# Optimization experiments

Hardware: AMD Instinct MI355X
Metric: run time of the kernel (lower is better)

## Reference

```python
import jax, jax.numpy as jnp
import numpy as np
from jax import lax

EPS = 1e-5
NUM_HEADS = 8


def _safe_norm(x):
    # sqrt(max(sum x^2, EPS^2)) == max(||x||, EPS); grad-safe at 0
    return jnp.sqrt(jnp.maximum(jnp.sum(x * x, axis=-1, keepdims=True), EPS * EPS))


def _project(x):
    norm = _safe_norm(x)
    max_norm = 1.0 - EPS
    scale = jnp.where(norm >= max_norm, max_norm / (norm + EPS), jnp.ones_like(norm))
    return x * scale


def _logmap0(y):
    # logarithmic_map(0, y): lambda_0 = 2/(1+EPS)
    y = _project(y)
    n = _safe_norm(y)  # clamp(min=EPS) is built in
    lam = 2.0 / (1.0 + EPS)
    return (2.0 / lam) * jnp.arctanh(n) * (y / n)


def _expmap0(v):
    # exponential_map(0, v): lambda_0 = 2/(1+EPS)
    n = _safe_norm(v)
    lam = 2.0 / (1.0 + EPS)
    return _project(jnp.tanh(lam * n / 2.0) * (v / n))


def _mobius_add(x, y):
    x = _project(x)
    y = _project(y)
    xy = jnp.sum(x * y, axis=-1, keepdims=True)
    xn = jnp.sum(x * x, axis=-1, keepdims=True)
    yn = jnp.sum(y * y, axis=-1, keepdims=True)
    num = (1.0 + 2.0 * xy + yn) * x + (1.0 - xn) * y
    den = 1.0 + 2.0 * xy + xn * yn + EPS
    return _project(num / den)


def _hyp_linear(x, W, b):
    # HyperbolicLinear.forward: project -> logmap0 -> linear -> expmap0 -> mobius-add bias
    x = _project(x)
    xt = _logmap0(x)
    t = xt @ W.T
    r = _expmap0(t)
    r = _mobius_add(r, jnp.broadcast_to(b, r.shape))
    return r


def setup_inputs() -> dict:
    key = jax.random.key(0)
    ks = jax.random.split(key, 11)
    B, S, E = 4, 512, 512

    def xavier(k, shape):
        bound = np.sqrt(6.0 / (shape[0] + shape[1]))
        return jax.random.uniform(k, shape, jnp.float32, -bound, bound)

    return {
        "query": jax.random.normal(ks[0], (B, S, E), jnp.float32),
        "key": jax.random.normal(ks[1], (B, S, E), jnp.float32),
        "value": jax.random.normal(ks[2], (B, S, E), jnp.float32),
        "Wq": xavier(ks[3], (E, E)), "bq": 0.01 * jax.random.normal(ks[4], (E,), jnp.float32),
        "Wk": xavier(ks[5], (E, E)), "bk": 0.01 * jax.random.normal(ks[6], (E,), jnp.float32),
        "Wv": xavier(ks[7], (E, E)), "bv": 0.01 * jax.random.normal(ks[8], (E,), jnp.float32),
        "Wo": xavier(ks[9], (E, E)), "bo": 0.01 * jax.random.normal(ks[10], (E,), jnp.float32),
    }


def reference(query, key, value, Wq, bq, Wk, bk, Wv, bv, Wo, bo):
    B, S, E = query.shape
    H = NUM_HEADS
    D = E // H

    Q = _hyp_linear(query, Wq, bq).reshape(B, S, H, D).transpose(0, 2, 1, 3)  # [B,H,S,D]
    K = _hyp_linear(key, Wk, bk).reshape(B, S, H, D).transpose(0, 2, 1, 3)
    V = _hyp_linear(value, Wv, bv).reshape(B, S, H, D).transpose(0, 2, 1, 3)

    # Pairwise Poincare distance: d(q,k) = acosh(1 + 2||q-k||^2/((1-|q|^2)(1-|k|^2)) + EPS)
    q = _project(Q)
    k = _project(K)
    qn = jnp.sum(q * q, axis=-1)  # [B,H,S]
    kn = jnp.sum(k * k, axis=-1)  # [B,H,S]
    qk = jnp.einsum('bhqd,bhkd->bhqk', q, k)
    num = jnp.maximum(qn[..., :, None] + kn[..., None, :] - 2.0 * qk, 0.0)
    den = jnp.maximum((1.0 - qn)[..., :, None] * (1.0 - kn)[..., None, :], EPS)
    dist = jnp.arccosh(1.0 + 2.0 * num / den + EPS)  # [B,H,Sq,Sk]
    attn = jax.nn.softmax(-dist, axis=-1)

    # Sequential Mobius-add accumulation over key/value positions
    wt = jnp.moveaxis(attn, 3, 0)  # [Sk,B,H,Sq]
    vt = jnp.moveaxis(V, 2, 0)     # [Sk,B,H,D]

    @jax.checkpoint
    def step(ws, wv):
        wj, vj = wv  # wj: [B,H,Sq], vj: [B,H,D]
        return _mobius_add(ws, wj[..., None] * vj[:, :, None, :]), None

    ws0 = jnp.zeros((B, H, S, D), query.dtype)
    attended, _ = lax.scan(step, ws0, (wt, vt))  # [B,H,Sq,D]

    attended = attended.transpose(0, 2, 1, 3).reshape(B, S, E)
    return _hyp_linear(attended, Wo, bo)
```

## Files before the change

kernel.cpp:

```cpp
#include <hip/hip_runtime.h>
#include <math.h>

#define EPS  1e-5f
#define EPS2 1e-10f
#define MAXN (1.0f - EPS)

using short8  = __attribute__((ext_vector_type(8))) short;
using floatx4 = __attribute__((ext_vector_type(4))) float;
using float2v = __attribute__((ext_vector_type(2))) float;

template <int CTRL>
static __device__ __forceinline__ float qperm(float x) {
  return __int_as_float(__builtin_amdgcn_update_dpp(
      __float_as_int(x), __float_as_int(x), CTRL, 0xF, 0xF, false));
}
#define QP_XOR1    0xB1
#define QP_XOR2    0x4E
#define QP_HALFMIR 0x141

#if __has_builtin(__builtin_elementwise_fma)
static __device__ __forceinline__ float2v fma2(float2v a, float2v b, float2v c) {
  return __builtin_elementwise_fma(a, b, c);
}
#else
static __device__ __forceinline__ float2v fma2(float2v a, float2v b, float2v c) {
  float2v r; r.x = fmaf(a.x, b.x, c.x); r.y = fmaf(a.y, b.y, c.y); return r;
}
#endif

static __device__ __forceinline__ int pack_hi2(float a, float b) {
  return (int)((__float_as_uint(a) >> 16) | (__float_as_uint(b) & 0xFFFF0000u));
}
static __device__ __forceinline__ float hi_of(float a) {
  return __uint_as_float(__float_as_uint(a) & 0xFFFF0000u);
}

static __device__ __forceinline__ float logmap_f(float ss) {
  const float r = sqrtf(fmaxf(ss, EPS2));
  float at;
  if (r >= MAXN) {
    at = 0.5f * logf((r * (2.0f - EPS) + EPS) / (EPS * (1.0f + r)));
  } else {
    at = 0.5f * logf((1.0f + r) / (1.0f - r));
  }
  return (1.0f + EPS) * at / r;
}

__global__ __launch_bounds__(256) void k_gemm_mfma(
    const float* __restrict__ A0, const float* __restrict__ A1, const float* __restrict__ A2,
    const float* __restrict__ W0, const float* __restrict__ W1, const float* __restrict__ W2,
    float* __restrict__ Cbase) {
  const int z = blockIdx.z;
  const float* A = (z == 0) ? A0 : ((z == 1) ? A1 : A2);
  const float* W = (z == 0) ? W0 : ((z == 1) ? W1 : W2);
  float* C = Cbase + (size_t)z * (2048 * 512);
  __shared__ int Ahi[64][36], Alo[64][36], Whi[64][36], Wlo[64][36];
  __shared__ float f_lds[64];
  const int t = threadIdx.x;
  const int n0 = blockIdx.x * 64;
  const int m0 = blockIdx.y * 64;
  const int row = t >> 2, c0 = (t & 3) * 16, ci = (t & 3) * 8;
  const int w = t >> 6, lane = t & 63;
  const int quad = lane >> 4, l16 = lane & 15;
  const int mw = (w & 1) * 32, nw = (w >> 1) * 32;
  floatx4 acc[2][2];
#pragma unroll
  for (int i = 0; i < 2; ++i)
#pragma unroll
    for (int j = 0; j < 2; ++j) acc[i][j] = (floatx4){0.f, 0.f, 0.f, 0.f};
  float ssq = 0.0f;

  for (int k0 = 0; k0 < 512; k0 += 64) {
    float4 av[4], wv[4];
#pragma unroll
    for (int i = 0; i < 4; ++i) {
      av[i] = *(const float4*)&A[(size_t)(n0 + row) * 512 + k0 + c0 + 4 * i];
      wv[i] = *(const float4*)&W[(size_t)(m0 + row) * 512 + k0 + c0 + 4 * i];
    }
    int pAh[8], pAl[8], pWh[8], pWl[8];
#pragma unroll
    for (int i = 0; i < 4; ++i) {
      ssq = fmaf(av[i].x, av[i].x, ssq); ssq = fmaf(av[i].y, av[i].y, ssq);
      ssq = fmaf(av[i].z, av[i].z, ssq); ssq = fmaf(av[i].w, av[i].w, ssq);
      pAh[2 * i]     = pack_hi2(av[i].x, av[i].y);
      pAh[2 * i + 1] = pack_hi2(av[i].z, av[i].w);
      pAl[2 * i]     = pack_hi2(av[i].x - hi_of(av[i].x), av[i].y - hi_of(av[i].y));
      pAl[2 * i + 1] = pack_hi2(av[i].z - hi_of(av[i].z), av[i].w - hi_of(av[i].w));
      pWh[2 * i]     = pack_hi2(wv[i].x, wv[i].y);
      pWh[2 * i + 1] = pack_hi2(wv[i].z, wv[i].w);
      pWl[2 * i]     = pack_hi2(wv[i].x - hi_of(wv[i].x), wv[i].y - hi_of(wv[i].y));
      pWl[2 * i + 1] = pack_hi2(wv[i].z - hi_of(wv[i].z), wv[i].w - hi_of(wv[i].w));
    }
    __syncthreads();
    *(int4*)&Ahi[row][ci]     = *(int4*)&pAh[0];
    *(int4*)&Ahi[row][ci + 4] = *(int4*)&pAh[4];
    *(int4*)&Alo[row][ci]     = *(int4*)&pAl[0];
    *(int4*)&Alo[row][ci + 4] = *(int4*)&pAl[4];
    *(int4*)&Whi[row][ci]     = *(int4*)&pWh[0];
    *(int4*)&Whi[row][ci + 4] = *(int4*)&pWh[4];
    *(int4*)&Wlo[row][ci]     = *(int4*)&pWl[0];
    *(int4*)&Wlo[row][ci + 4] = *(int4*)&pWl[4];
    __syncthreads();
#pragma unroll
    for (int kk = 0; kk < 64; kk += 32) {
      short8 ah[2], al[2], bh[2], bl[2];
#pragma unroll
      for (int i = 0; i < 2; ++i) {
        ah[i] = *(const short8*)&((const short*)Ahi[mw + i * 16 + l16])[kk + quad * 8];
        al[i] = *(const short8*)&((const short*)Alo[mw + i * 16 + l16])[kk + quad * 8];
        bh[i] = *(const short8*)&((const short*)Whi[nw + i * 16 + l16])[kk + quad * 8];
        bl[i] = *(const short8*)&((const short*)Wlo[nw + i * 16 + l16])[kk + quad * 8];
      }
#pragma unroll
      for (int i = 0; i < 2; ++i)
#pragma unroll
        for (int j = 0; j < 2; ++j) {
          acc[i][j] = __builtin_amdgcn_mfma_f32_16x16x32_bf16(ah[i], bh[j], acc[i][j], 0, 0, 0);
          acc[i][j] = __builtin_amdgcn_mfma_f32_16x16x32_bf16(ah[i], bl[j], acc[i][j], 0, 0, 0);
          acc[i][j] = __builtin_amdgcn_mfma_f32_16x16x32_bf16(al[i], bh[j], acc[i][j], 0, 0, 0);
        }
    }
  }
  ssq += qperm<QP_XOR1>(ssq);
  ssq += qperm<QP_XOR2>(ssq);
  if ((t & 3) == 0) f_lds[row] = logmap_f(ssq);
  __syncthreads();
#pragma unroll
  for (int i = 0; i < 2; ++i) {
    const int lrow_base = mw + i * 16 + quad * 4;
#pragma unroll
    for (int r = 0; r < 4; ++r) {
      const float fv = f_lds[lrow_base + r];
#pragma unroll
      for (int j = 0; j < 2; ++j)
        C[(size_t)(n0 + lrow_base + r) * 512 + m0 + nw + j * 16 + l16] = fv * acc[i][j][r];
    }
  }
}

__global__ __launch_bounds__(256) void k_post(const float* __restrict__ tin,
                                              const float* __restrict__ b0,
                                              const float* __restrict__ b1,
                                              const float* __restrict__ b2,
                                              float* __restrict__ o0, float* __restrict__ o1,
                                              float* __restrict__ o2,
                                              float* __restrict__ nrm0, float* __restrict__ nrm1,
                                              float* __restrict__ nrm2,
                                              float* __restrict__ rowsum_init, int final_mode) {
  const int nrow = blockIdx.x, z = blockIdx.y, t = threadIdx.x;
  const float* tv = tin + ((size_t)z * 2048 + nrow) * 512;
  const float* bias = (z == 0) ? b0 : ((z == 1) ? b1 : b2);
  const int e0 = 2 * t;
  const float2 tp = *(const float2*)&tv[e0];
  const float2 bp = *(const float2*)&bias[e0];
  float p_tt = tp.x * tp.x + tp.y * tp.y;
  float p_tb = tp.x * bp.x + tp.y * bp.y;
  float p_bb = bp.x * bp.x + bp.y * bp.y;
#pragma unroll
  for (int m = 32; m; m >>= 1) {
    p_tt += __shfl_xor(p_tt, m, 64);
    p_tb += __shfl_xor(p_tb, m, 64);
    p_bb += __shfl_xor(p_bb, m, 64);
  }
  __shared__ float red[4][3];
  const int lane = t & 63, w = t >> 6;
  if (lane == 0) { red[w][0] = p_tt; red[w][1] = p_tb; red[w][2] = p_bb; }
  __syncthreads();
  const float s_tt = red[0][0] + red[1][0] + red[2][0] + red[3][0];
  const float s_tb = red[0][1] + red[1][1] + red[2][1] + red[3][1];
  const float s_bb = red[0][2] + red[1][2] + red[2][2] + red[3][2];
  const float tn = sqrtf(fmaxf(s_tt, EPS2));
  const float th = tanhf(tn / (1.0f + EPS));
  const float g = th / tn;
  const float rnorm = th * (sqrtf(s_tt) / tn);
  const float sr = (rnorm >= MAXN) ? (MAXN / (rnorm + EPS)) : 1.0f;
  const float gr = g * sr;
  const float rn = (rnorm * sr) * (rnorm * sr);
  const float bnorm = sqrtf(fmaxf(s_bb, EPS2));
  const float sb = (bnorm >= MAXN) ? (MAXN / (bnorm + EPS)) : 1.0f;
  const float xy = gr * sb * s_tb;
  const float yn = (sb * sb) * s_bb;
  const float Af = 1.0f + 2.0f * xy + yn;
  const float Cf = 1.0f - rn;
  const float den = 1.0f + 2.0f * xy + rn * yn + EPS;
  const float id = 1.0f / den;
  const float on_raw = (Af * Af * rn + 2.0f * Af * Cf * xy + Cf * Cf * yn) * (id * id);
  const float no = sqrtf(fmaxf(on_raw, EPS2));
  const float so = (no >= MAXN) ? (MAXN / (no + EPS)) : 1.0f;
  const float ms = id * so;
  const float ca = gr * Af * ms;
  const float cb = sb * Cf * ms;
  const float v0 = ca * tp.x + cb * bp.x;
  const float v1 = ca * tp.y + cb * bp.y;
  if (final_mode) {
    float2 o; o.x = v0; o.y = v1;
    *(float2*)&o0[(size_t)nrow * 512 + e0] = o;
    return;
  }
  float hp = v0 * v0 + v1 * v1;
#pragma unroll
  for (int m = 16; m; m >>= 1) hp += __shfl_xor(hp, m, 64);
  const float hnr = sqrtf(fmaxf(hp, EPS2));
  float sh = 1.0f;
  if (z != 2) sh = (hnr >= MAXN) ? (MAXN / (hnr + EPS)) : 1.0f;
  float* outz = (z == 0) ? o0 : ((z == 1) ? o1 : o2);
  float* nz = (z == 0) ? nrm0 : ((z == 1) ? nrm1 : nrm2);
  const int b = nrow >> 9, s = nrow & 511, h = e0 >> 6, d = e0 & 63;
  float2 o; o.x = v0 * sh; o.y = v1 * sh;
  *(float2*)&outz[(((size_t)(b * 8 + h) * 512 + s) * 64 + d)] = o;
  if ((t & 31) == 0) nz[(size_t)(b * 8 + h) * 512 + s] = hp * sh * sh;
  if (z == 0 && t < 8) rowsum_init[((size_t)(nrow >> 9) * 8 + t) * 512 + (nrow & 511)] = 0.0f;
}

__global__ __launch_bounds__(256) void k_logits(const float* __restrict__ Q,
                                                const float* __restrict__ K,
                                                const float* __restrict__ qn,
                                                const float* __restrict__ kn,
                                                float* __restrict__ attn,
                                                float* __restrict__ rowsum) {
  const int bh = blockIdx.z;
  const int i0 = blockIdx.x * 64;
  const int j0 = blockIdx.y * 64;
  const float* Qb = Q + (size_t)bh * 512 * 64;
  const float* Kb = K + (size_t)bh * 512 * 64;
  __shared__ int Qhi[64][36], Qlo[64][36], Khi[64][36], Klo[64][36];
  const int t = threadIdx.x;
  const int row = t >> 2, c0 = (t & 3) * 16, ci = (t & 3) * 8;
  const int w = t >> 6, lane = t & 63;
  const int quad = lane >> 4, l16 = lane & 15;
  const int mw = (w & 1) * 32, nw = (w >> 1) * 32;
  float4 qv4[4], kv4[4];
#pragma unroll
  for (int i = 0; i < 4; ++i) {
    qv4[i] = *(const float4*)&Qb[(size_t)(i0 + row) * 64 + c0 + 4 * i];
    kv4[i] = *(const float4*)&Kb[(size_t)(j0 + row) * 64 + c0 + 4 * i];
  }
  int pQh[8], pQl[8], pKh[8], pKl[8];
#pragma unroll
  for (int i = 0; i < 4; ++i) {
    pQh[2 * i]     = pack_hi2(qv4[i].x, qv4[i].y);
    pQh[2 * i + 1] = pack_hi2(qv4[i].z, qv4[i].w);
    pQl[2 * i]     = pack_hi2(qv4[i].x - hi_of(qv4[i].x), qv4[i].y - hi_of(qv4[i].y));
    pQl[2 * i + 1] = pack_hi2(qv4[i].z - hi_of(qv4[i].z), qv4[i].w - hi_of(qv4[i].w));
    pKh[2 * i]     = pack_hi2(kv4[i].x, kv4[i].y);
    pKh[2 * i + 1] = pack_hi2(kv4[i].z, kv4[i].w);
    pKl[2 * i]     = pack_hi2(kv4[i].x - hi_of(kv4[i].x), kv4[i].y - hi_of(kv4[i].y));
    pKl[2 * i + 1] = pack_hi2(kv4[i].z - hi_of(kv4[i].z), kv4[i].w - hi_of(kv4[i].w));
  }
  *(int4*)&Qhi[row][ci]     = *(int4*)&pQh[0];
  *(int4*)&Qhi[row][ci + 4] = *(int4*)&pQh[4];
  *(int4*)&Qlo[row][ci]     = *(int4*)&pQl[0];
  *(int4*)&Qlo[row][ci + 4] = *(int4*)&pQl[4];
  *(int4*)&Khi[row][ci]     = *(int4*)&pKh[0];
  *(int4*)&Khi[row][ci + 4] = *(int4*)&pKh[4];
  *(int4*)&Klo[row][ci]     = *(int4*)&pKl[0];
  *(int4*)&Klo[row][ci + 4] = *(int4*)&pKl[4];
  __syncthreads();
  floatx4 acc[2][2];
#pragma unroll
  for (int i = 0; i < 2; ++i)
#pragma unroll
    for (int j = 0; j < 2; ++j) acc[i][j] = (floatx4){0.f, 0.f, 0.f, 0.f};
#pragma unroll
  for (int kk = 0; kk < 64; kk += 32) {
    short8 ah[2], al[2], bhv[2], blv[2];
#pragma unroll
    for (int i = 0; i < 2; ++i) {
      ah[i]  = *(const short8*)&((const short*)Qhi[mw + i * 16 + l16])[kk + quad * 8];
      al[i]  = *(const short8*)&((const short*)Qlo[mw + i * 16 + l16])[kk + quad * 8];
      bhv[i] = *(const short8*)&((const short*)Khi[nw + i * 16 + l16])[kk + quad * 8];
      blv[i] = *(const short8*)&((const short*)Klo[nw + i * 16 + l16])[kk + quad * 8];
    }
#pragma unroll
    for (int i = 0; i < 2; ++i)
#pragma unroll
      for (int j = 0; j < 2; ++j) {
        acc[i][j] = __builtin_amdgcn_mfma_f32_16x16x32_bf16(ah[i], bhv[j], acc[i][j], 0, 0, 0);
        acc[i][j] = __builtin_amdgcn_mfma_f32_16x16x32_bf16(ah[i], blv[j], acc[i][j], 0, 0, 0);
        acc[i][j] = __builtin_amdgcn_mfma_f32_16x16x32_bf16(al[i], bhv[j], acc[i][j], 0, 0, 0);
      }
  }
#pragma unroll
  for (int i = 0; i < 2; ++i) {
    float rs_acc[4] = {0.f, 0.f, 0.f, 0.f};
#pragma unroll
    for (int r = 0; r < 4; ++r) {
      const int grow = i0 + mw + i * 16 + quad * 4 + r;
      const float qni = qn[(size_t)bh * 512 + grow];
      const float rq = 1.0f - qni;
#pragma unroll
      for (int j = 0; j < 2; ++j) {
        const int gcol = j0 + nw + j * 16 + l16;
        const float knj = kn[(size_t)bh * 512 + gcol];
        const float num = fmaxf(qni + knj - 2.0f * acc[i][j][r], 0.0f);
        const float den = fmaxf(rq * (1.0f - knj), EPS);
        const float wv = fmaf(2.0f * num, __builtin_amdgcn_rcpf(den), EPS);
        const float s_ = 1.0f + wv + sqrtf(wv * (wv + 2.0f));
        const float rr = __builtin_amdgcn_rcpf(s_);
        rs_acc[r] += rr;
        attn[((size_t)bh * 512 + grow) * 512 + gcol] = rr;
      }
    }
#pragma unroll
    for (int r = 0; r < 4; ++r) {
      float v = rs_acc[r];
      v += __shfl_xor(v, 1, 64); v += __shfl_xor(v, 2, 64);
      v += __shfl_xor(v, 4, 64); v += __shfl_xor(v, 8, 64);
      if (l16 == 0)
        atomicAdd(&rowsum[(size_t)bh * 512 + i0 + mw + i * 16 + quad * 4 + r], v);
    }
  }
}

__global__ __launch_bounds__(256) void k_scan(const float* __restrict__ V,
                                              const float* __restrict__ vn,
                                              const float* __restrict__ rw,
                                              const float* __restrict__ rowsum,
                                              float* __restrict__ att) {
  __shared__ __align__(16) float v_lds[64 * 64];
  __shared__ __align__(16) float swyn_lds[64 * 66];
  __shared__ float g_lds[64];
  const int blk = blockIdx.x;
  const int bh = blk >> 4;
  const int i0 = (blk & 15) * 32;
  const int t = threadIdx.x;
  const int lane = t & 63, w = t >> 6;
  const int row_blk = w * 8 + (lane >> 3);
  const int sub = lane & 7;
  const int d0 = sub * 8;
  const float* Vb = V + (size_t)bh * 512 * 64;
  const float* vnb = vn + (size_t)bh * 512;
  const float* arow = rw + ((size_t)bh * 512 + i0 + row_blk) * 512;
  const float inv_s = __builtin_amdgcn_rcpf(rowsum[(size_t)bh * 512 + i0 + row_blk]);

  float2v wsv[4];
#pragma unroll
  for (int k = 0; k < 4; ++k) wsv[k] = (float2v){0.f, 0.f};
  float xn = 0.0f;

  for (int jc = 0; jc < 512; jc += 64) {
#pragma unroll
    for (int it = 0; it < 4; ++it) {
      const int idx4 = it * 256 + t;
      *(float4*)&v_lds[idx4 * 4] = *(const float4*)&Vb[(size_t)jc * 64 + idx4 * 4];
    }
    const float4 a0 = *(const float4*)&arow[jc + sub * 8];
    const float4 a1 = *(const float4*)&arow[jc + sub * 8 + 4];
    const float4 n0 = *(const float4*)&vnb[jc + sub * 8];
    const float4 n1 = *(const float4*)&vnb[jc + sub * 8 + 4];
    const float wq[8] = {a0.x, a0.y, a0.z, a0.w, a1.x, a1.y, a1.z, a1.w};
    const float nq[8] = {n0.x, n0.y, n0.z, n0.w, n1.x, n1.y, n1.z, n1.w};
#pragma unroll
    for (int e = 0; e < 8; ++e) {
      const float wgt = wq[e] * inv_s;
      float2 p; p.x = wgt; p.y = (wgt * wgt) * nq[e];
      *(float2*)&swyn_lds[(sub * 8 + e) * 66 + row_blk * 2] = p;
    }
    __syncthreads();

    {
      const int jg = row_blk * 2;
      const float4 va0 = *(const float4*)&v_lds[jg * 64 + d0];
      const float4 va1 = *(const float4*)&v_lds[jg * 64 + d0 + 4];
      const float4 vb0 = *(const float4*)&v_lds[(jg + 1) * 64 + d0];
      const float4 vb1 = *(const float4*)&v_lds[(jg + 1) * 64 + d0 + 4];
      const float4 vc0 = *(const float4*)&v_lds[((jg + 2) & 63) * 64 + d0];
      const float4 vc1 = *(const float4*)&v_lds[((jg + 2) & 63) * 64 + d0 + 4];
      float p0 = va0.x * vb0.x + va0.y * vb0.y + va0.z * vb0.z + va0.w * vb0.w +
                 va1.x * vb1.x + va1.y * vb1.y + va1.z * vb1.z + va1.w * vb1.w;
      float p1 = vb0.x * vc0.x + vb0.y * vc0.y + vb0.z * vc0.z + vb0.w * vc0.w +
                 vb1.x * vc1.x + vb1.y * vc1.y + vb1.z * vc1.z + vb1.w * vc1.w;
      p0 += qperm<QP_XOR1>(p0); p0 += qperm<QP_XOR2>(p0); p0 += qperm<QP_HALFMIR>(p0);
      p1 += qperm<QP_XOR1>(p1); p1 += qperm<QP_XOR2>(p1); p1 += qperm<QP_HALFMIR>(p1);
      if (sub == 0) { g_lds[jg] = p0; g_lds[jg + 1] = p1; }
    }
    float2v vcur[4];
    {
      const float4 c0v = *(const float4*)&v_lds[d0];
      const float4 c1v = *(const float4*)&v_lds[d0 + 4];
      vcur[0] = (float2v){c0v.x, c0v.y}; vcur[1] = (float2v){c0v.z, c0v.w};
      vcur[2] = (float2v){c1v.x, c1v.y}; vcur[3] = (float2v){c1v.z, c1v.w};
    }
    float2v dd = wsv[0] * vcur[0];
    dd = fma2(wsv[1], vcur[1], dd);
    dd = fma2(wsv[2], vcur[2], dd);
    dd = fma2(wsv[3], vcur[3], dd);
    float D = dd.x + dd.y;
    D += qperm<QP_XOR1>(D); D += qperm<QP_XOR2>(D); D += qperm<QP_HALFMIR>(D);
    __syncthreads();

#pragma unroll
    for (int j = 0; j < 64; ++j) {
      const float2 sy2 = *(const float2*)&swyn_lds[j * 66 + row_blk * 2];
      const float sw = sy2.x, yn = sy2.y;
      const float xnyn1 = fmaf(xn, yn, 1.0f + EPS);
      const float sxy   = xn + yn;
      const float ynp1  = 1.0f + yn;
      const float Cfsw  = (1.0f - xn) * sw;
      float2v vnx[4];
      float E = 0.0f;
      if (j < 63) {
        const float4 nx0 = *(const float4*)&v_lds[(j + 1) * 64 + d0];
        const float4 nx1 = *(const float4*)&v_lds[(j + 1) * 64 + d0 + 4];
        vnx[0] = (float2v){nx0.x, nx0.y}; vnx[1] = (float2v){nx0.z, nx0.w};
        vnx[2] = (float2v){nx1.x, nx1.y}; vnx[3] = (float2v){nx1.z, nx1.w};
        float2v ee = wsv[0] * vnx[0];
        ee = fma2(wsv[1], vnx[1], ee);
        ee = fma2(wsv[2], vnx[2], ee);
        ee = fma2(wsv[3], vnx[3], ee);
        E = ee.x + ee.y;
        E += qperm<QP_XOR1>(E); E += qperm<QP_XOR2>(E); E += qperm<QP_HALFMIR>(E);
      }
      const float xy  = sw * D;
      const float den = fmaf(2.0f, xy, xnyn1);
      const float s2  = fmaf(2.0f, xy, sxy);
      const float Af  = fmaf(2.0f, xy, ynp1);
      const float id  = __builtin_amdgcn_rcpf(den);
      const float dn  = den - EPS;
      const float am  = Af * id;
      const float cm  = Cfsw * id;
      xn = (s2 * id) * (dn * id);
      const float2v amv = {am, am};
      const float2v cmv = {cm, cm};
      wsv[0] = fma2(amv, wsv[0], cmv * vcur[0]);
      wsv[1] = fma2(amv, wsv[1], cmv * vcur[1]);
      wsv[2] = fma2(amv, wsv[2], cmv * vcur[2]);
      wsv[3] = fma2(amv, wsv[3], cmv * vcur[3]);
      if (j < 63) {
        D = fmaf(am, E, cm * g_lds[j]);
        vcur[0] = vnx[0]; vcur[1] = vnx[1]; vcur[2] = vnx[2]; vcur[3] = vnx[3];
      }
    }
    __syncthreads();
  }
  const int b = bh >> 3, h = bh & 7;
  float* o = att + (((size_t)b * 512 + i0 + row_blk) * 512 + h * 64 + d0);
  float4 s0; s0.x = wsv[0].x; s0.y = wsv[0].y; s0.z = wsv[1].x; s0.w = wsv[1].y;
  float4 s1; s1.x = wsv[2].x; s1.y = wsv[2].y; s1.z = wsv[3].x; s1.w = wsv[3].y;
  *(float4*)&o[0] = s0;
  *(float4*)&o[4] = s1;
}

extern "C" void kernel_launch(void* const* d_in, const int* in_sizes, int n_in,
                              void* d_out, int out_size, void* d_ws, size_t ws_size,
                              hipStream_t stream) {
  const float* query = (const float*)d_in[0];
  const float* key_  = (const float*)d_in[1];
  const float* value = (const float*)d_in[2];
  const float* Wq = (const float*)d_in[3];
  const float* bq = (const float*)d_in[4];
  const float* Wk = (const float*)d_in[5];
  const float* bk = (const float*)d_in[6];
  const float* Wv = (const float*)d_in[7];
  const float* bv = (const float*)d_in[8];
  const float* Wo = (const float*)d_in[9];
  const float* bo = (const float*)d_in[10];
  float* ws = (float*)d_ws;
  const size_t M = 1u << 20;
  float* Qb     = ws;
  float* Kb     = ws + 1 * M;
  float* Vb     = ws + 2 * M;
  float* qn     = ws + 3 * M;
  float* kn     = qn + 16384;
  float* vn     = kn + 16384;
  float* rowsum = vn + 16384;
  float* rw     = ws + 4 * M;
  float* t3     = ws + 12 * M;
  float* att    = ws + 15 * M;
  float* to_    = ws + 16 * M;

  k_gemm_mfma<<<dim3(32, 8, 3), 256, 0, stream>>>(query, key_, value, Wq, Wk, Wv, t3);
  k_post<<<dim3(2048, 3), 256, 0, stream>>>(t3, bq, bk, bv, Qb, Kb, Vb, qn, kn, vn,
                                            rowsum, 0);
  k_logits<<<dim3(8, 8, 32), 256, 0, stream>>>(Qb, Kb, qn, kn, rw, rowsum);
  k_scan<<<512, 256, 0, stream>>>(Vb, vn, rw, rowsum, att);
  k_gemm_mfma<<<dim3(32, 8, 1), 256, 0, stream>>>(att, att, att, Wo, Wo, Wo, to_);
  k_post<<<dim3(2048, 1), 256, 0, stream>>>(to_, bo, bo, bo, (float*)d_out,
                                            nullptr, nullptr, nullptr, nullptr, nullptr,
                                            nullptr, 1);
}
```

Measured before the change: 239.9 us.

## Fuse all six stages into one cooperative persistent kernel with grid syncs

Replaces the six separate kernel launches with a single cooperative kernel of 512 blocks. Each stage runs as a grid-stride loop over its original block indices, stages are separated by grid.sync, and one shared-memory buffer is reused across stages. This removes per-launch overhead and the gaps between kernels. In exchange, occupancy is capped by the largest stage's shared memory, the grid is fixed at 512 blocks, grid-wide barriers are added, and correctness depends on all blocks being co-resident.

```diff
diff --git a/kernel.cpp b/kernel.cpp
--- a/kernel.cpp
+++ b/kernel.cpp
@@ -1,5 +1,8 @@
 #include <hip/hip_runtime.h>
+#include <hip/hip_cooperative_groups.h>
 #include <math.h>
+
+namespace cg = cooperative_groups;
 
 #define EPS  1e-5f
 #define EPS2 1e-10f
@@ -46,19 +49,14 @@
   return (1.0f + EPS) * at / r;
 }
 
-__global__ __launch_bounds__(256) void k_gemm_mfma(
-    const float* __restrict__ A0, const float* __restrict__ A1, const float* __restrict__ A2,
-    const float* __restrict__ W0, const float* __restrict__ W1, const float* __restrict__ W2,
-    float* __restrict__ Cbase) {
-  const int z = blockIdx.z;
-  const float* A = (z == 0) ? A0 : ((z == 1) ? A1 : A2);
-  const float* W = (z == 0) ? W0 : ((z == 1) ? W1 : W2);
-  float* C = Cbase + (size_t)z * (2048 * 512);
-  __shared__ int Ahi[64][36], Alo[64][36], Whi[64][36], Wlo[64][36];
-  __shared__ float f_lds[64];
+struct SGemm { int Ahi[64][36]; int Alo[64][36]; int Whi[64][36]; int Wlo[64][36]; float f_lds[64]; };
+struct SLog  { int Qhi[64][36]; int Qlo[64][36]; int Khi[64][36]; int Klo[64][36]; };
+struct SScan { float v_lds[64 * 64]; float swyn[64 * 66]; float g[64]; };
+struct SPost { float red[4][3]; };
+
+static __device__ void gemm_body(const float* __restrict__ A, const float* __restrict__ W,
+                                 float* __restrict__ C, int n0, int m0, SGemm* S) {
   const int t = threadIdx.x;
-  const int n0 = blockIdx.x * 64;
-  const int m0 = blockIdx.y * 64;
   const int row = t >> 2, c0 = (t & 3) * 16, ci = (t & 3) * 8;
   const int w = t >> 6, lane = t & 63;
   const int quad = lane >> 4, l16 = lane & 15;
@@ -92,24 +90,24 @@
       pWl[2 * i + 1] = pack_hi2(wv[i].z - hi_of(wv[i].z), wv[i].w - hi_of(wv[i].w));
     }
     __syncthreads();
-    *(int4*)&Ahi[row][ci]     = *(int4*)&pAh[0];
-    *(int4*)&Ahi[row][ci + 4] = *(int4*)&pAh[4];
-    *(int4*)&Alo[row][ci]     = *(int4*)&pAl[0];
-    *(int4*)&Alo[row][ci + 4] = *(int4*)&pAl[4];
-    *(int4*)&Whi[row][ci]     = *(int4*)&pWh[0];
-    *(int4*)&Whi[row][ci + 4] = *(int4*)&pWh[4];
-    *(int4*)&Wlo[row][ci]     = *(int4*)&pWl[0];
-    *(int4*)&Wlo[row][ci + 4] = *(int4*)&pWl[4];
+    *(int4*)&S->Ahi[row][ci]     = *(int4*)&pAh[0];
+    *(int4*)&S->Ahi[row][ci + 4] = *(int4*)&pAh[4];
+    *(int4*)&S->Alo[row][ci]     = *(int4*)&pAl[0];
+    *(int4*)&S->Alo[row][ci + 4] = *(int4*)&pAl[4];
+    *(int4*)&S->Whi[row][ci]     = *(int4*)&pWh[0];
+    *(int4*)&S->Whi[row][ci + 4] = *(int4*)&pWh[4];
+    *(int4*)&S->Wlo[row][ci]     = *(int4*)&pWl[0];
+    *(int4*)&S->Wlo[row][ci + 4] = *(int4*)&pWl[4];
     __syncthreads();
 #pragma unroll
     for (int kk = 0; kk < 64; kk += 32) {
       short8 ah[2], al[2], bh[2], bl[2];
 #pragma unroll
       for (int i = 0; i < 2; ++i) {
-        ah[i] = *(const short8*)&((const short*)Ahi[mw + i * 16 + l16])[kk + quad * 8];
-        al[i] = *(const short8*)&((const short*)Alo[mw + i * 16 + l16])[kk + quad * 8];
-        bh[i] = *(const short8*)&((const short*)Whi[nw + i * 16 + l16])[kk + quad * 8];
-        bl[i] = *(const short8*)&((const short*)Wlo[nw + i * 16 + l16])[kk + quad * 8];
+        ah[i] = *(const short8*)&((const short*)S->Ahi[mw + i * 16 + l16])[kk + quad * 8];
+        al[i] = *(const short8*)&((const short*)S->Alo[mw + i * 16 + l16])[kk + quad * 8];
+        bh[i] = *(const short8*)&((const short*)S->Whi[nw + i * 16 + l16])[kk + quad * 8];
+        bl[i] = *(const short8*)&((const short*)S->Wlo[nw + i * 16 + l16])[kk + quad * 8];
       }
 #pragma unroll
       for (int i = 0; i < 2; ++i)
@@ -123,14 +121,14 @@
   }
   ssq += qperm<QP_XOR1>(ssq);
   ssq += qperm<QP_XOR2>(ssq);
-  if ((t & 3) == 0) f_lds[row] = logmap_f(ssq);
+  if ((t & 3) == 0) S->f_lds[row] = logmap_f(ssq);
   __syncthreads();
 #pragma unroll
   for (int i = 0; i < 2; ++i) {
     const int lrow_base = mw + i * 16 + quad * 4;
 #pragma unroll
     for (int r = 0; r < 4; ++r) {
-      const float fv = f_lds[lrow_base + r];
+      const float fv = S->f_lds[lrow_base + r];
 #pragma unroll
       for (int j = 0; j < 2; ++j)
         C[(size_t)(n0 + lrow_base + r) * 512 + m0 + nw + j * 16 + l16] = fv * acc[i][j][r];
@@ -138,16 +136,15 @@
   }
 }
 
-__global__ __launch_bounds__(256) void k_post(const float* __restrict__ tin,
-                                              const float* __restrict__ b0,
-                                              const float* __restrict__ b1,
-                                              const float* __restrict__ b2,
-                                              float* __restrict__ o0, float* __restrict__ o1,
-                                              float* __restrict__ o2,
-                                              float* __restrict__ nrm0, float* __restrict__ nrm1,
-                                              float* __restrict__ nrm2,
-                                              float* __restrict__ rowsum_init, int final_mode) {
-  const int nrow = blockIdx.x, z = blockIdx.y, t = threadIdx.x;
+static __device__ void post_body(const float* __restrict__ tin,
+                                 const float* __restrict__ b0, const float* __restrict__ b1,
+                                 const float* __restrict__ b2,
+                                 float* __restrict__ o0, float* __restrict__ o1,
+                                 float* __restrict__ o2,
+                                 float* __restrict__ nrm0, float* __restrict__ nrm1,
+                                 float* __restrict__ nrm2, float* __restrict__ rowsum_init,
+                                 int nrow, int z, int final_mode, SPost* S) {
+  const int t = threadIdx.x;
   const float* tv = tin + ((size_t)z * 2048 + nrow) * 512;
   const float* bias = (z == 0) ? b0 : ((z == 1) ? b1 : b2);
   const int e0 = 2 * t;
@@ -162,13 +159,12 @@
     p_tb += __shfl_xor(p_tb, m, 64);
     p_bb += __shfl_xor(p_bb, m, 64);
   }
-  __shared__ float red[4][3];
   const int lane = t & 63, w = t >> 6;
-  if (lane == 0) { red[w][0] = p_tt; red[w][1] = p_tb; red[w][2] = p_bb; }
+  if (lane == 0) { S->red[w][0] = p_tt; S->red[w][1] = p_tb; S->red[w][2] = p_bb; }
   __syncthreads();
-  const float s_tt = red[0][0] + red[1][0] + red[2][0] + red[3][0];
-  const float s_tb = red[0][1] + red[1][1] + red[2][1] + red[3][1];
-  const float s_bb = red[0][2] + red[1][2] + red[2][2] + red[3][2];
+  const float s_tt = S->red[0][0] + S->red[1][0] + S->red[2][0] + S->red[3][0];
+  const float s_tb = S->red[0][1] + S->red[1][1] + S->red[2][1] + S->red[3][1];
+  const float s_bb = S->red[0][2] + S->red[1][2] + S->red[2][2] + S->red[3][2];
   const float tn = sqrtf(fmaxf(s_tt, EPS2));
   const float th = tanhf(tn / (1.0f + EPS));
   const float g = th / tn;
@@ -195,35 +191,31 @@
   if (final_mode) {
     float2 o; o.x = v0; o.y = v1;
     *(float2*)&o0[(size_t)nrow * 512 + e0] = o;
-    return;
-  }
-  float hp = v0 * v0 + v1 * v1;
-#pragma unroll
-  for (int m = 16; m; m >>= 1) hp += __shfl_xor(hp, m, 64);
-  const float hnr = sqrtf(fmaxf(hp, EPS2));
-  float sh = 1.0f;
-  if (z != 2) sh = (hnr >= MAXN) ? (MAXN / (hnr + EPS)) : 1.0f;
-  float* outz = (z == 0) ? o0 : ((z == 1) ? o1 : o2);
-  float* nz = (z == 0) ? nrm0 : ((z == 1) ? nrm1 : nrm2);
-  const int b = nrow >> 9, s = nrow & 511, h = e0 >> 6, d = e0 & 63;
-  float2 o; o.x = v0 * sh; o.y = v1 * sh;
-  *(float2*)&outz[(((size_t)(b * 8 + h) * 512 + s) * 64 + d)] = o;
-  if ((t & 31) == 0) nz[(size_t)(b * 8 + h) * 512 + s] = hp * sh * sh;
-  if (z == 0 && t < 8) rowsum_init[((size_t)(nrow >> 9) * 8 + t) * 512 + (nrow & 511)] = 0.0f;
-}
-
-__global__ __launch_bounds__(256) void k_logits(const float* __restrict__ Q,
-                                                const float* __restrict__ K,
-                                                const float* __restrict__ qn,
-                                                const float* __restrict__ kn,
-                                                float* __restrict__ attn,
-                                                float* __restrict__ rowsum) {
-  const int bh = blockIdx.z;
-  const int i0 = blockIdx.x * 64;
-  const int j0 = blockIdx.y * 64;
+  } else {
+    float hp = v0 * v0 + v1 * v1;
+#pragma unroll
+    for (int m = 16; m; m >>= 1) hp += __shfl_xor(hp, m, 64);
+    const float hnr = sqrtf(fmaxf(hp, EPS2));
+    float sh = 1.0f;
+    if (z != 2) sh = (hnr >= MAXN) ? (MAXN / (hnr + EPS)) : 1.0f;
+    float* outz = (z == 0) ? o0 : ((z == 1) ? o1 : o2);
+    float* nz = (z == 0) ? nrm0 : ((z == 1) ? nrm1 : nrm2);
+    const int b = nrow >> 9, s = nrow & 511, h = e0 >> 6, d = e0 & 63;
+    float2 o; o.x = v0 * sh; o.y = v1 * sh;
+    *(float2*)&outz[(((size_t)(b * 8 + h) * 512 + s) * 64 + d)] = o;
+    if ((t & 31) == 0) nz[(size_t)(b * 8 + h) * 512 + s] = hp * sh * sh;
+    if (z == 0 && t < 8) rowsum_init[((size_t)(nrow >> 9) * 8 + t) * 512 + (nrow & 511)] = 0.0f;
+  }
+}
+
+static __device__ void logits_body(const float* __restrict__ Q, const float* __restrict__ K,
+                                   const float* __restrict__ qn, const float* __restrict__ kn,
+                                   float* __restrict__ attn, float* __restrict__ rowsum,
+                                   int xb, int yb, int bh, SLog* S) {
+  const int i0 = xb * 64;
+  const int j0 = yb * 64;
   const float* Qb = Q + (size_t)bh * 512 * 64;
   const float* Kb = K + (size_t)bh * 512 * 64;
-  __shared__ int Qhi[64][36], Qlo[64][36], Khi[64][36], Klo[64][36];
   const int t = threadIdx.x;
   const int row = t >> 2, c0 = (t & 3) * 16, ci = (t & 3) * 8;
   const int w = t >> 6, lane = t & 63;
@@ -247,14 +239,15 @@
     pKl[2 * i]     = pack_hi2(kv4[i].x - hi_of(kv4[i].x), kv4[i].y - hi_of(kv4[i].y));
     pKl[2 * i + 1] = pack_hi2(kv4[i].z - hi_of(kv4[i].z), kv4[i].w - hi_of(kv4[i].w));
   }
-  *(int4*)&Qhi[row][ci]     = *(int4*)&pQh[0];
-  *(int4*)&Qhi[row][ci + 4] = *(int4*)&pQh[4];
-  *(int4*)&Qlo[row][ci]     = *(int4*)&pQl[0];
-  *(int4*)&Qlo[row][ci + 4] = *(int4*)&pQl[4];
-  *(int4*)&Khi[row][ci]     = *(int4*)&pKh[0];
-  *(int4*)&Khi[row][ci + 4] = *(int4*)&pKh[4];
-  *(int4*)&Klo[row][ci]     = *(int4*)&pKl[0];
-  *(int4*)&Klo[row][ci + 4] = *(int4*)&pKl[4];
+  __syncthreads();
+  *(int4*)&S->Qhi[row][ci]     = *(int4*)&pQh[0];
+  *(int4*)&S->Qhi[row][ci + 4] = *(int4*)&pQh[4];
+  *(int4*)&S->Qlo[row][ci]     = *(int4*)&pQl[0];
+  *(int4*)&S->Qlo[row][ci + 4] = *(int4*)&pQl[4];
+  *(int4*)&S->Khi[row][ci]     = *(int4*)&pKh[0];
+  *(int4*)&S->Khi[row][ci + 4] = *(int4*)&pKh[4];
+  *(int4*)&S->Klo[row][ci]     = *(int4*)&pKl[0];
+  *(int4*)&S->Klo[row][ci + 4] = *(int4*)&pKl[4];
   __syncthreads();
   floatx4 acc[2][2];
 #pragma unroll
@@ -266,10 +259,10 @@
     short8 ah[2], al[2], bhv[2], blv[2];
 #pragma unroll
     for (int i = 0; i < 2; ++i) {
-      ah[i]  = *(const short8*)&((const short*)Qhi[mw + i * 16 + l16])[kk + quad * 8];
-      al[i]  = *(const short8*)&((const short*)Qlo[mw + i * 16 + l16])[kk + quad * 8];
-      bhv[i] = *(const short8*)&((const short*)Khi[nw + i * 16 + l16])[kk + quad * 8];
-      blv[i] = *(const short8*)&((const short*)Klo[nw + i * 16 + l16])[kk + quad * 8];
+      ah[i]  = *(const short8*)&((const short*)S->Qhi[mw + i * 16 + l16])[kk + quad * 8];
+      al[i]  = *(const short8*)&((const short*)S->Qlo[mw + i * 16 + l16])[kk + quad * 8];
+      bhv[i] = *(const short8*)&((const short*)S->Khi[nw + i * 16 + l16])[kk + quad * 8];
+      blv[i] = *(const short8*)&((const short*)S->Klo[nw + i * 16 + l16])[kk + quad * 8];
     }
 #pragma unroll
     for (int i = 0; i < 2; ++i)
@@ -312,15 +305,9 @@
   }
 }
 
-__global__ __launch_bounds__(256) void k_scan(const float* __restrict__ V,
-                                              const float* __restrict__ vn,
-                                              const float* __restrict__ rw,
-                                              const float* __restrict__ rowsum,
-                                              float* __restrict__ att) {
-  __shared__ __align__(16) float v_lds[64 * 64];
-  __shared__ __align__(16) float swyn_lds[64 * 66];
-  __shared__ float g_lds[64];
-  const int blk = blockIdx.x;
+static __device__ void scan_body(const float* __restrict__ V, const float* __restrict__ vn,
+                                 const float* __restrict__ rw, const float* __restrict__ rowsum,
+                                 float* __restrict__ att, int blk, SScan* S) {
   const int bh = blk >> 4;
   const int i0 = (blk & 15) * 32;
   const int t = threadIdx.x;
@@ -342,7 +329,7 @@
 #pragma unroll
     for (int it = 0; it < 4; ++it) {
       const int idx4 = it * 256 + t;
-      *(float4*)&v_lds[idx4 * 4] = *(const float4*)&Vb[(size_t)jc * 64 + idx4 * 4];
+      *(float4*)&S->v_lds[idx4 * 4] = *(const float4*)&Vb[(size_t)jc * 64 + idx4 * 4];
     }
     const float4 a0 = *(const float4*)&arow[jc + sub * 8];
     const float4 a1 = *(const float4*)&arow[jc + sub * 8 + 4];
@@ -354,30 +341,30 @@
     for (int e = 0; e < 8; ++e) {
       const float wgt = wq[e] * inv_s;
       float2 p; p.x = wgt; p.y = (wgt * wgt) * nq[e];
-      *(float2*)&swyn_lds[(sub * 8 + e) * 66 + row_blk * 2] = p;
+      *(float2*)&S->swyn[(sub * 8 + e) * 66 + row_blk * 2] = p;
     }
     __syncthreads();
 
     {
       const int jg = row_blk * 2;
-      const float4 va0 = *(const float4*)&v_lds[jg * 64 + d0];
-      const float4 va1 = *(const float4*)&v_lds[jg * 64 + d0 + 4];
-      const float4 vb0 = *(const float4*)&v_lds[(jg + 1) * 64 + d0];
-      const float4 vb1 = *(const float4*)&v_lds[(jg + 1) * 64 + d0 + 4];
-      const float4 vc0 = *(const float4*)&v_lds[((jg + 2) & 63) * 64 + d0];
-      const float4 vc1 = *(const float4*)&v_lds[((jg + 2) & 63) * 64 + d0 + 4];
+      const float4 va0 = *(const float4*)&S->v_lds[jg * 64 + d0];
+      const float4 va1 = *(const float4*)&S->v_lds[jg * 64 + d0 + 4];
+      const float4 vb0 = *(const float4*)&S->v_lds[(jg + 1) * 64 + d0];
+      const float4 vb1 = *(const float4*)&S->v_lds[(jg + 1) * 64 + d0 + 4];
+      const float4 vc0 = *(const float4*)&S->v_lds[((jg + 2) & 63) * 64 + d0];
+      const float4 vc1 = *(const float4*)&S->v_lds[((jg + 2) & 63) * 64 + d0 + 4];
       float p0 = va0.x * vb0.x + va0.y * vb0.y + va0.z * vb0.z + va0.w * vb0.w +
                  va1.x * vb1.x + va1.y * vb1.y + va1.z * vb1.z + va1.w * vb1.w;
       float p1 = vb0.x * vc0.x + vb0.y * vc0.y + vb0.z * vc0.z + vb0.w * vc0.w +
                  vb1.x * vc1.x + vb1.y * vc1.y + vb1.z * vc1.z + vb1.w * vc1.w;
       p0 += qperm<QP_XOR1>(p0); p0 += qperm<QP_XOR2>(p0); p0 += qperm<QP_HALFMIR>(p0);
       p1 += qperm<QP_XOR1>(p1); p1 += qperm<QP_XOR2>(p1); p1 += qperm<QP_HALFMIR>(p1);
-      if (sub == 0) { g_lds[jg] = p0; g_lds[jg + 1] = p1; }
+      if (sub == 0) { S->g[jg] = p0; S->g[jg + 1] = p1; }
     }
     float2v vcur[4];
     {
-      const float4 c0v = *(const float4*)&v_lds[d0];
-      const float4 c1v = *(const float4*)&v_lds[d0 + 4];
+      const float4 c0v = *(const float4*)&S->v_lds[d0];
+      const float4 c1v = *(const float4*)&S->v_lds[d0 + 4];
       vcur[0] = (float2v){c0v.x, c0v.y}; vcur[1] = (float2v){c0v.z, c0v.w};
       vcur[2] = (float2v){c1v.x, c1v.y}; vcur[3] = (float2v){c1v.z, c1v.w};
     }
@@ -391,7 +378,7 @@
 
 #pragma unroll
     for (int j = 0; j < 64; ++j) {
-      const float2 sy2 = *(const float2*)&swyn_lds[j * 66 + row_blk * 2];
+      const float2 sy2 = *(const float2*)&S->swyn[j * 66 + row_blk * 2];
       const float sw = sy2.x, yn = sy2.y;
       const float xnyn1 = fmaf(xn, yn, 1.0f + EPS);
       const float sxy   = xn + yn;
@@ -400,8 +387,8 @@
       float2v vnx[4];
       float E = 0.0f;
       if (j < 63) {
-        const float4 nx0 = *(const float4*)&v_lds[(j + 1) * 64 + d0];
-        const float4 nx1 = *(const float4*)&v_lds[(j + 1) * 64 + d0 + 4];
+        const float4 nx0 = *(const float4*)&S->v_lds[(j + 1) * 64 + d0];
+        const float4 nx1 = *(const float4*)&S->v_lds[(j + 1) * 64 + d0 + 4];
         vnx[0] = (float2v){nx0.x, nx0.y}; vnx[1] = (float2v){nx0.z, nx0.w};
         vnx[2] = (float2v){nx1.x, nx1.y}; vnx[3] = (float2v){nx1.z, nx1.w};
         float2v ee = wsv[0] * vnx[0];
@@ -427,7 +414,7 @@
       wsv[2] = fma2(amv, wsv[2], cmv * vcur[2]);
       wsv[3] = fma2(amv, wsv[3], cmv * vcur[3]);
       if (j < 63) {
-        D = fmaf(am, E, cm * g_lds[j]);
+        D = fmaf(am, E, cm * S->g[j]);
         vcur[0] = vnx[0]; vcur[1] = vnx[1]; vcur[2] = vnx[2]; vcur[3] = vnx[3];
       }
     }
@@ -439,6 +426,57 @@
   float4 s1; s1.x = wsv[2].x; s1.y = wsv[2].y; s1.z = wsv[3].x; s1.w = wsv[3].y;
   *(float4*)&o[0] = s0;
   *(float4*)&o[4] = s1;
+}
+
+__global__ __launch_bounds__(256, 2) void k_mega(
+    const float* query, const float* key_, const float* value,
+    const float* Wq, const float* bq, const float* Wk, const float* bk,
+    const float* Wv, const float* bv, const float* Wo, const float* bo,
+    float* Qb, float* Kb, float* Vb, float* qn, float* kn, float* vnrm,
+    float* rowsum, float* rw, float* t3, float* att, float* to_, float* out) {
+  __shared__ __align__(16) char smem_raw[sizeof(SGemm)];
+  cg::grid_group grid = cg::this_grid();
+  const int bid = blockIdx.x;
+
+  for (int v = bid; v < 768; v += 512) {
+    const int z = v >> 8, rem = v & 255;
+    const float* A = (z == 0) ? query : ((z == 1) ? key_ : value);
+    const float* W = (z == 0) ? Wq : ((z == 1) ? Wk : Wv);
+    gemm_body(A, W, t3 + (size_t)z * (2048 * 512), (rem & 31) * 64, (rem >> 5) * 64,
+              (SGemm*)smem_raw);
+    __syncthreads();
+  }
+  grid.sync();
+
+  for (int v = bid; v < 6144; v += 512) {
+    post_body(t3, bq, bk, bv, Qb, Kb, Vb, qn, kn, vnrm, rowsum,
+              v & 2047, v >> 11, 0, (SPost*)smem_raw);
+    __syncthreads();
+  }
+  grid.sync();
+
+  for (int v = bid; v < 2048; v += 512) {
+    logits_body(Qb, Kb, qn, kn, rw, rowsum, v & 7, (v >> 3) & 7, v >> 6,
+                (SLog*)smem_raw);
+    __syncthreads();
+  }
+  __threadfence();
+  grid.sync();
+
+  scan_body(Vb, vnrm, rw, rowsum, att, bid, (SScan*)smem_raw);
+  grid.sync();
+
+  for (int v = bid; v < 256; v += 512) {
+    gemm_body(att, Wo, to_, (v & 31) * 64, (v >> 5) * 64, (SGemm*)smem_raw);
+    __syncthreads();
+  }
+  grid.sync();
+
+  for (int v = bid; v < 2048; v += 512) {
+    post_body(to_, bo, bo, bo, out, nullptr, nullptr, nullptr, nullptr, nullptr,
+              nullptr, v, 0, 1, (SPost*)smem_raw);
+    __syncthreads();
+  }
 }
 
 extern "C" void kernel_launch(void* const* d_in, const int* in_sizes, int n_in,
@@ -468,14 +506,14 @@
   float* t3     = ws + 12 * M;
   float* att    = ws + 15 * M;
   float* to_    = ws + 16 * M;
-
-  k_gemm_mfma<<<dim3(32, 8, 3), 256, 0, stream>>>(query, key_, value, Wq, Wk, Wv, t3);
-  k_post<<<dim3(2048, 3), 256, 0, stream>>>(t3, bq, bk, bv, Qb, Kb, Vb, qn, kn, vn,
-                                            rowsum, 0);
-  k_logits<<<dim3(8, 8, 32), 256, 0, stream>>>(Qb, Kb, qn, kn, rw, rowsum);
-  k_scan<<<512, 256, 0, stream>>>(Vb, vn, rw, rowsum, att);
-  k_gemm_mfma<<<dim3(32, 8, 1), 256, 0, stream>>>(att, att, att, Wo, Wo, Wo, to_);
-  k_post<<<dim3(2048, 1), 256, 0, stream>>>(to_, bo, bo, bo, (float*)d_out,
-                                            nullptr, nullptr, nullptr, nullptr, nullptr,
-                                            nullptr, 1);
-}
+  float* out    = (float*)d_out;
+
+  void* args[] = {
+    (void*)&query, (void*)&key_, (void*)&value,
+    (void*)&Wq, (void*)&bq, (void*)&Wk, (void*)&bk,
+    (void*)&Wv, (void*)&bv, (void*)&Wo, (void*)&bo,
+    (void*)&Qb, (void*)&Kb, (void*)&Vb, (void*)&qn, (void*)&kn, (void*)&vn,
+    (void*)&rowsum, (void*)&rw, (void*)&t3, (void*)&att, (void*)&to_, (void*)&out,
+  };
+  hipLaunchCooperativeKernel((const void*)k_mega, dim3(512), dim3(256), args, 0, stream);
+}
```

Result: slower. 610.6 us (+154.6%).
